# Performance work log

Measured on AMD Instinct MI355X. Metric: run time of the kernel, lower is better.

The kernel has to match this reference:

```python
import jax, jax.numpy as jnp
import numpy as np

NC, K, SD = 8, 1024, 64
L = NC * SD
B = 8192
TAU = 0.07
COMMIT_W = 1.0
CONTRAST_W = 1.0
EPS = 1e-12


def setup_inputs() -> dict:
    key = jax.random.key(0)
    kz, ke = jax.random.split(key)
    z = jax.random.normal(kz, (B, L), dtype=jnp.float32)
    embeddings = jax.random.normal(ke, (NC, K, SD), dtype=jnp.float32)
    return {"z": z, "embeddings": embeddings}


def reference(z, embeddings):
    sg = jax.lax.stop_gradient
    Bn, Ln = z.shape
    nc, k, sd = embeddings.shape
    zr = z.reshape(Bn, nc, sd)  # (B, nc, sd)

    # squared distances via ||z||^2 - 2 z.e + ||e||^2 -> (B, nc, K), avoids (B,nc,K,sd)
    z2 = jnp.sum(zr * zr, axis=-1)[:, :, None]
    e2 = jnp.sum(embeddings * embeddings, axis=-1)[None, :, :]
    cross = jnp.einsum('bnd,nkd->bnk', zr, embeddings)
    dists = z2 - 2.0 * cross + e2
    indices = jnp.argmin(dists, axis=-1)  # (B, nc)

    # codebook gather
    quant_splits = embeddings[jnp.arange(nc)[None, :], indices]  # (B, nc, sd)
    quant_z = quant_splits.reshape(Bn, Ln)

    commit_loss = jnp.mean((sg(quant_z) - z) ** 2)
    embed_loss = jnp.mean((quant_z - sg(z)) ** 2)
    total_commit = commit_loss + embed_loss

    quant_z_st = z + sg(quant_z - z)

    z_norm = z / jnp.maximum(jnp.linalg.norm(z, axis=-1, keepdims=True), EPS)
    q_det = sg(quant_z)
    q_norm = q_det / jnp.maximum(jnp.linalg.norm(q_det, axis=-1, keepdims=True), EPS)
    logits = jnp.matmul(q_norm, z_norm.T) / TAU  # (B, B)
    # cross-entropy with labels = arange(B)
    contrastive = jnp.mean(jax.nn.logsumexp(logits, axis=1) - jnp.diagonal(logits))

    return (quant_z_st, COMMIT_W * total_commit, CONTRAST_W * contrastive, indices)
```

## Files before the change

kernel.cpp:

```cpp
#include <hip/hip_runtime.h>
#include <cstdint>
#include <cstddef>

#define NCB   8
#define KC    1024
#define SDIM  64
#define LDIM  512
#define BATCH 8192
#define INV_TAU (1.0f/0.07f)
#define K2E  20.60992915555662f
#define DBIAS 256.0f

typedef __bf16 bf16_t;
typedef bf16_t bf16x8 __attribute__((ext_vector_type(8)));
typedef float  floatx4 __attribute__((ext_vector_type(4)));
typedef int    intx8  __attribute__((ext_vector_type(8)));
typedef unsigned int u32;

__device__ __forceinline__ unsigned short f2bf(float f) {
    union { float f; unsigned int u; } c; c.f = f;
    unsigned int u = c.u;
    u += 0x7fffu + ((u >> 16) & 1u);
    return (unsigned short)(u >> 16);
}
__device__ __forceinline__ float bf2f(unsigned short h) {
    union { unsigned int u; float f; } c; c.u = ((unsigned int)h) << 16;
    return c.f;
}
__device__ __forceinline__ float exp2_fast(float x) {
    float r; asm("v_exp_f32 %0, %1" : "=v"(r) : "v"(x)); return r;
}
__device__ __forceinline__ void gll16(const void* g, void* l) {
    __builtin_amdgcn_global_load_lds(
        (const __attribute__((address_space(1))) u32*)g,
        (__attribute__((address_space(3))) u32*)l,
        16, 0, 0);
}

__global__ __launch_bounds__(256) void
k_pre(const float* __restrict__ emb, float* __restrict__ e2,
      unsigned short* __restrict__ eh, unsigned short* __restrict__ el,
      float* __restrict__ accs) {
    int id = blockIdx.x * 256 + threadIdx.x;
    const float4* e4 = (const float4*)(emb + (size_t)id * SDIM);
    ushort4* eh4 = (ushort4*)(eh + (size_t)id * SDIM);
    ushort4* el4 = (ushort4*)(el + (size_t)id * SDIM);
    float s0=0.f,s1=0.f,s2=0.f,s3=0.f;
#pragma unroll
    for (int i=0;i<16;i++){ float4 v=e4[i];
        s0=fmaf(v.x,v.x,s0); s1=fmaf(v.y,v.y,s1);
        s2=fmaf(v.z,v.z,s2); s3=fmaf(v.w,v.w,s3);
        ushort4 h, l;
        h.x=f2bf(v.x); l.x=f2bf(v.x-bf2f(h.x));
        h.y=f2bf(v.y); l.y=f2bf(v.y-bf2f(h.y));
        h.z=f2bf(v.z); l.z=f2bf(v.z-bf2f(h.z));
        h.w=f2bf(v.w); l.w=f2bf(v.w-bf2f(h.w));
        eh4[i]=h; el4[i]=l;
    }
    e2[id] = (s0+s1)+(s2+s3);
    if (id==0){ accs[0]=0.f; accs[1]=0.f; accs[2]=0.f; }
}

__device__ __forceinline__ double dist64d(const float* __restrict__ e,
                                          const float* __restrict__ zg) {
    double se=0.0, sz=0.0;
#pragma unroll 8
    for (int i=0;i<64;i++){ double ev=(double)e[i];
        se = fma(ev,ev,se); sz = fma(ev,(double)zg[i],sz); }
    return se - 2.0*sz;
}

__global__ __launch_bounds__(256,3) void
k_argmin(const unsigned short* __restrict__ eh, const unsigned short* __restrict__ el,
         const float* __restrict__ e2, const float* __restrict__ z,
         const float* __restrict__ emb, float* __restrict__ out_q,
         float* __restrict__ out_idx, float* __restrict__ accs) {
    __shared__ __align__(16) unsigned short Bh[2][64*64], Bl[2][64*64];
    __shared__ unsigned int mK[2][128][2];

    const int tid = threadIdx.x;
    const int n   = blockIdx.y;
    const int i0  = blockIdx.x * 128;
    const int wid = tid >> 6, lane = tid & 63;
    const int wm = wid & 1, wn = wid >> 1;
    const int c  = lane & 15, qq = lane >> 4;

    const unsigned char* ehb = (const unsigned char*)(eh + (size_t)n*KC*SDIM);
    const unsigned char* elb = (const unsigned char*)(el + (size_t)n*KC*SDIM);
    const float* e2n = e2 + n*KC;

    const int brow = lane >> 3;
    const int bchk = ((lane & 7)*16) ^ (brow << 4);

    auto stageB = [&](int buf, int j0){
#pragma unroll
        for (int s=0;s<2;s++){
            int r0 = wid*16 + s*8;
            size_t go = (size_t)(j0 + r0 + brow)*128 + bchk;
            gll16(ehb + go, &Bh[buf][r0*64]);
            gll16(elb + go, &Bl[buf][r0*64]);
        }
    };

    stageB(0, 0);

    bf16x8 ah[4][2], al[4][2];
#pragma unroll
    for (int mt=0;mt<4;mt++)
#pragma unroll
        for (int t=0;t<2;t++){
            const float* zr = z + (size_t)(i0 + wm*64 + mt*16 + c)*LDIM
                                + n*SDIM + t*32 + qq*8;
            float4 v0 = *(const float4*)(zr);
            float4 v1 = *(const float4*)(zr + 4);
            ushort4 h0, l0, h1, l1;
            h0.x=f2bf(v0.x); l0.x=f2bf(v0.x-bf2f(h0.x));
            h0.y=f2bf(v0.y); l0.y=f2bf(v0.y-bf2f(h0.y));
            h0.z=f2bf(v0.z); l0.z=f2bf(v0.z-bf2f(h0.z));
            h0.w=f2bf(v0.w); l0.w=f2bf(v0.w-bf2f(h0.w));
            h1.x=f2bf(v1.x); l1.x=f2bf(v1.x-bf2f(h1.x));
            h1.y=f2bf(v1.y); l1.y=f2bf(v1.y-bf2f(h1.y));
            h1.z=f2bf(v1.z); l1.z=f2bf(v1.z-bf2f(h1.z));
            h1.w=f2bf(v1.w); l1.w=f2bf(v1.w-bf2f(h1.w));
            union { bf16x8 v; ushort4 u[2]; } uh, ul;
            uh.u[0]=h0; uh.u[1]=h1; ul.u[0]=l0; ul.u[1]=l1;
            ah[mt][t]=uh.v; al[mt][t]=ul.v;
        }

    unsigned int k1[16], k2[16];
#pragma unroll
    for (int j=0;j<16;j++){ k1[j]=0xFFFFFFFFu; k2[j]=0xFFFFFFFFu; }

    __syncthreads();

    for (int jt=0; jt<16; jt++){
        const int cur = jt & 1, nxt = cur ^ 1;
        const int j0 = jt*64;
        if (jt < 15) stageB(nxt, j0 + 64);

        float e2v[2];
#pragma unroll
        for (int nt=0;nt<2;nt++)
            e2v[nt] = e2n[j0 + wn*32 + nt*16 + c] + DBIAS;

        floatx4 acc[4][2];
#pragma unroll
        for (int mt=0;mt<4;mt++){
            acc[mt][0]=(floatx4){0.f,0.f,0.f,0.f};
            acc[mt][1]=(floatx4){0.f,0.f,0.f,0.f};
        }

#pragma unroll
        for (int t=0;t<2;t++){
            const int axo = (t*32 + qq*8) ^ ((c&7)<<3);
            bf16x8 bh[2], bl[2];
#pragma unroll
            for (int nt=0;nt<2;nt++){
                int ro = (wn*32 + nt*16 + c)*64 + axo;
                bh[nt] = *(const bf16x8*)(&Bh[cur][ro]);
                bl[nt] = *(const bf16x8*)(&Bl[cur][ro]);
            }
#pragma unroll
            for (int mt=0;mt<4;mt++)
#pragma unroll
                for (int nt=0;nt<2;nt++){
                    acc[mt][nt] = __builtin_amdgcn_mfma_f32_16x16x32_bf16(ah[mt][t], bh[nt], acc[mt][nt], 0,0,0);
                    acc[mt][nt] = __builtin_amdgcn_mfma_f32_16x16x32_bf16(ah[mt][t], bl[nt], acc[mt][nt], 0,0,0);
                    acc[mt][nt] = __builtin_amdgcn_mfma_f32_16x16x32_bf16(al[mt][t], bh[nt], acc[mt][nt], 0,0,0);
                }
        }

#pragma unroll
        for (int nt=0;nt<2;nt++){
            const int colb = wn*32 + nt*16 + c;
            unsigned int kidx = (unsigned int)(j0 + colb);
#pragma unroll
            for (int mt=0;mt<4;mt++)
#pragma unroll
                for (int reg=0;reg<4;reg++){
                    float d = fmaf(-2.0f, acc[mt][nt][reg], e2v[nt]);
                    unsigned int key = (__float_as_uint(d) & 0xFFFFFC00u) | kidx;
                    int s = mt*4+reg;
                    unsigned int o1 = k1[s], o2 = k2[s];
                    unsigned int nk2;
                    asm("v_med3_u32 %0, %1, %2, %3" : "=v"(nk2) : "v"(o1), "v"(o2), "v"(key));
                    k2[s] = nk2;
                    k1[s] = min(o1, key);
                }
        }
        __syncthreads();
    }

#pragma unroll
    for (int off=1; off<16; off<<=1){
#pragma unroll
        for (int s=0;s<16;s++){
            unsigned int o1 = __shfl_xor(k1[s], off);
            unsigned int o2 = __shfl_xor(k2[s], off);
            unsigned int n1 = min(k1[s], o1);
            k2[s] = min( max(k1[s], o1), min(k2[s], o2) );
            k1[s] = n1;
        }
    }
    if (c == 0){
#pragma unroll
        for (int s=0;s<16;s++){
            int row = wm*64 + (s>>2)*16 + qq*4 + (s&3);
            mK[wn][row][0] = k1[s]; mK[wn][row][1] = k2[s];
        }
    }
    __syncthreads();

    if (tid < 128){
        int b = i0 + tid;
        unsigned int a1 = mK[0][tid][0], a2 = mK[0][tid][1];
        unsigned int c1 = mK[1][tid][0], c2 = mK[1][tid][1];
        unsigned int f1 = min(a1, c1);
        unsigned int f2 = min( max(a1, c1), min(a2, c2) );
        int ii1 = (int)(f1 & 0x3FFu);
        int ii2 = (int)(f2 & 0x3FFu);
        float d1q = __uint_as_float(f1 & 0xFFFFFC00u);
        float d2q = __uint_as_float(f2 & 0xFFFFFC00u);

        const float* eb = emb + (size_t)n*KC*SDIM;
        const float* zg = z + (size_t)b*LDIM + n*SDIM;
        if (d2q - d1q < 0.08f) {
            double d1 = dist64d(eb + (size_t)ii1*SDIM, zg);
            double d2 = dist64d(eb + (size_t)ii2*SDIM, zg);
            if (d2 < d1 || (d2 == d1 && ii2 < ii1)) ii1 = ii2;
        }

        const float4* q4 = (const float4*)(eb + (size_t)ii1*SDIM);
        const float4* z4 = (const float4*)zg;
        float4* oq = (float4*)(out_q + (size_t)b*LDIM + n*SDIM);
        float cs = 0.f;
#pragma unroll
        for (int i=0;i<16;i++){
            float4 v = q4[i]; float4 zv = z4[i];
            oq[i] = v;
            float d0=v.x-zv.x, d1=v.y-zv.y, d2=v.z-zv.z, d3=v.w-zv.w;
            cs += d0*d0 + d1*d1 + d2*d2 + d3*d3;
        }
        out_idx[b*NCB + n] = (float)ii1;

        for (int off=32; off; off>>=1) cs += __shfl_down(cs, off);
        if ((tid & 63)==0) atomicAdd(&accs[0], cs);
    }
}

__global__ __launch_bounds__(256) void
k_norm(const float* __restrict__ z, const float* __restrict__ q,
       unsigned char* __restrict__ zn8, unsigned char* __restrict__ qn8,
       float* __restrict__ diag) {
    const int b = blockIdx.x, tid = threadIdx.x;
    const size_t base = (size_t)b*LDIM;
    float2 zv = ((const float2*)(z+base))[tid];
    float2 qv = ((const float2*)(q+base))[tid];
    float sz = zv.x*zv.x + zv.y*zv.y;
    float sq = qv.x*qv.x + qv.y*qv.y;
    float sqz= qv.x*zv.x + qv.y*zv.y;
    for (int off=32; off; off>>=1){
        sz+=__shfl_down(sz,off); sq+=__shfl_down(sq,off); sqz+=__shfl_down(sqz,off);
    }
    __shared__ float red[3][4];
    __shared__ float bc[2];
    int w = tid>>6;
    if ((tid&63)==0){ red[0][w]=sz; red[1][w]=sq; red[2][w]=sqz; }
    __syncthreads();
    if (tid==0){
        float tz = red[0][0]+red[0][1]+red[0][2]+red[0][3];
        float tq = red[1][0]+red[1][1]+red[1][2]+red[1][3];
        float tz_q = red[2][0]+red[2][1]+red[2][2]+red[2][3];
        float inz = 1.0f/fmaxf(sqrtf(tz), 1e-12f);
        float inq = 1.0f/fmaxf(sqrtf(tq), 1e-12f);
        bc[0]=inz; bc[1]=inq;
        diag[b] = tz_q*inz*inq*INV_TAU;
    }
    __syncthreads();
    float inz=bc[0], inq=bc[1];
    int pz = __builtin_amdgcn_cvt_pk_fp8_f32(zv.x*inz, zv.y*inz, 0, false);
    int pq = __builtin_amdgcn_cvt_pk_fp8_f32(qv.x*inq, qv.y*inq, 0, false);
    ((unsigned short*)(zn8+base))[tid] = (unsigned short)(pz & 0xffff);
    ((unsigned short*)(qn8+base))[tid] = (unsigned short)(pq & 0xffff);
}

__global__ __launch_bounds__(512,4) void
k_logits(const unsigned char* __restrict__ qn8, const unsigned char* __restrict__ zn8,
         float* __restrict__ Spart) {
    __shared__ __align__(16) unsigned char Bs[2][64*512];
    const int tid  = threadIdx.x;
    const int i0   = blockIdx.x * 128;
    const int chnk = blockIdx.y;
    const int wid  = tid >> 6, lane = tid & 63;
    const int wm = wid & 3, wn = wid >> 2;
    const int c  = lane & 15, qq = lane >> 4;

    const int brow  = lane >> 5;
    const int bchk0 = (lane & 31) * 16;

    auto stageB = [&](int buf, int j0){
#pragma unroll
        for (int s=0;s<4;s++){
            int r0  = wid*8 + s*2;
            int row = r0 + brow;
            gll16(zn8 + (size_t)(j0+row)*LDIM + (bchk0 ^ ((row&7)<<4)),
                  &Bs[buf][r0*512]);
        }
    };

    stageB(0, chnk*1024);

    intx8 af[2][4];
#pragma unroll
    for (int mt=0;mt<2;mt++){
        const unsigned char* ap = qn8 + (size_t)(i0 + wm*32 + mt*16 + c)*LDIM + qq*32;
#pragma unroll
        for (int kc=0;kc<4;kc++){
            union { intx8 v; uint4 h[2]; } u;
            u.h[0] = *(const uint4*)(ap + kc*128);
            u.h[1] = *(const uint4*)(ap + kc*128 + 16);
            af[mt][kc] = u.v;
        }
    }

    float S[8];
#pragma unroll
    for (int i=0;i<8;i++) S[i] = 0.f;

    __syncthreads();

    for (int jt=0;jt<16;jt++){
        const int cur = jt & 1;
        const int j0 = chnk*1024 + jt*64;
        if (jt < 15) stageB(cur^1, j0 + 64);

        floatx4 acc[2][2];
#pragma unroll
        for (int mt=0;mt<2;mt++){
            acc[mt][0]=(floatx4){0.f,0.f,0.f,0.f};
            acc[mt][1]=(floatx4){0.f,0.f,0.f,0.f};
        }

#pragma unroll
        for (int kc=0;kc<4;kc++){
            intx8 bfr[2];
#pragma unroll
            for (int nt=0;nt<2;nt++){
                const int rb = wn*32 + nt*16 + c;
                const unsigned char* p = &Bs[cur][rb*512];
                const int o = kc*128 + qq*32;
                const int x = (rb&7)<<4;
                union { intx8 v; uint4 h[2]; } u;
                u.h[0] = *(const uint4*)(p + (o ^ x));
                u.h[1] = *(const uint4*)(p + ((o + 16) ^ x));
                bfr[nt] = u.v;
            }
#pragma unroll
            for (int mt=0;mt<2;mt++)
#pragma unroll
                for (int nt=0;nt<2;nt++)
                    acc[mt][nt] = __builtin_amdgcn_mfma_scale_f32_16x16x128_f8f6f4(
                        af[mt][kc], bfr[nt], acc[mt][nt],
                        0, 0,
                        0, 127,
                        0, 127);
        }

#pragma unroll
        for (int mt=0;mt<2;mt++)
#pragma unroll
            for (int reg=0;reg<4;reg++){
                float e0 = exp2_fast(fmaf(acc[mt][0][reg], K2E, -K2E));
                float e1 = exp2_fast(fmaf(acc[mt][1][reg], K2E, -K2E));
                S[mt*4+reg] += e0 + e1;
            }
        __syncthreads();
    }

#pragma unroll
    for (int off=1; off<16; off<<=1)
#pragma unroll
        for (int s=0;s<8;s++) S[s] += __shfl_xor(S[s], off);

    if (c == 0){
        const int p = chnk*2 + wn;
#pragma unroll
        for (int mt=0;mt<2;mt++)
#pragma unroll
            for (int reg=0;reg<4;reg++){
                int row = i0 + wm*32 + mt*16 + qq*4 + reg;
                Spart[p*BATCH + row] = S[mt*4+reg];
            }
    }
}

__global__ __launch_bounds__(256) void
k_finalize(const float* __restrict__ Spart, const float* __restrict__ diag,
           float* __restrict__ accs, float* __restrict__ out_s) {
    int r = blockIdx.x*256 + threadIdx.x;
    float Ssum = 0.f;
#pragma unroll
    for (int p=0;p<16;p++) Ssum += Spart[p*BATCH + r];
    float val = INV_TAU + logf(Ssum) - diag[r];
    for (int off=32; off; off>>=1) val += __shfl_down(val, off);
    if ((threadIdx.x & 63)==0) atomicAdd(&accs[1], val);
    __syncthreads();
    if (threadIdx.x == 0){
        __threadfence();
        unsigned int old = __float_as_uint(atomicAdd(&accs[2], 1.0f));
        if (old == __float_as_uint(31.0f)) {
            __threadfence();
            float a0 = atomicAdd(&accs[0], 0.0f);
            float a1 = atomicAdd(&accs[1], 0.0f);
            out_s[0] = 2.0f*a0 / (float)((size_t)BATCH*LDIM);
            out_s[1] = a1 / (float)BATCH;
        }
    }
}

extern "C" void kernel_launch(void* const* d_in, const int* in_sizes, int n_in,
                              void* d_out, int out_size, void* d_ws, size_t ws_size,
                              hipStream_t stream) {
    const float* z   = (const float*)d_in[0];
    const float* emb = (const float*)d_in[1];
    float* out = (float*)d_out;
    float* out_q       = out;
    float* out_scalars = out + 4194304;
    float* out_idx     = out + 4194306;

    float* wsf   = (float*)d_ws;
    float* e2    = wsf;
    float* accs  = wsf + 8192;
    float* diag  = wsf + 8704;
    float* Spart = wsf + 16896;
    unsigned char* qn8 = (unsigned char*)(Spart + 32*BATCH);
    unsigned char* zn8 = qn8 + (size_t)BATCH*LDIM;
    unsigned short* eh = (unsigned short*)(zn8 + (size_t)BATCH*LDIM);
    unsigned short* el = eh + (size_t)NCB*KC*SDIM;

    k_pre    <<<32,          256, 0, stream>>>(emb, e2, eh, el, accs);
    k_argmin <<<dim3(64,8),  256, 0, stream>>>(eh, el, e2, z, emb,
                                               out_q, out_idx, accs);
    k_norm   <<<BATCH,       256, 0, stream>>>(z, out_q, zn8, qn8, diag);
    k_logits <<<dim3(64,8),  512, 0, stream>>>(qn8, zn8, Spart);
    k_finalize<<<32,         256, 0, stream>>>(Spart, diag, accs, out_scalars);
}
```

Before: 184.3 us.

## Restructure argmin, logits, norm and pre kernels for occupancy and parallelism

k_argmin now stages the z hi/lo bf16 split in shared memory instead of registers, uses 32-wide codebook tiles, and caches the e2 values in LDS. k_logits moves to 256-thread blocks with 32-row B tiles and one N-wave layout, which halves the partial sums that k_finalize has to read. k_norm processes one row per wave with wave-level shuffles, and k_pre spreads each embedding row over 8 threads. Together these aim to cut register pressure, raise occupancy, and spread the small kernels across more threads, at the cost of extra LDS reads for the A operand.

```diff
diff --git a/kernel.cpp b/kernel.cpp
--- a/kernel.cpp
+++ b/kernel.cpp
@@ -41,24 +41,26 @@
 k_pre(const float* __restrict__ emb, float* __restrict__ e2,
       unsigned short* __restrict__ eh, unsigned short* __restrict__ el,
       float* __restrict__ accs) {
-    int id = blockIdx.x * 256 + threadIdx.x;
-    const float4* e4 = (const float4*)(emb + (size_t)id * SDIM);
-    ushort4* eh4 = (ushort4*)(eh + (size_t)id * SDIM);
-    ushort4* el4 = (ushort4*)(el + (size_t)id * SDIM);
-    float s0=0.f,s1=0.f,s2=0.f,s3=0.f;
-#pragma unroll
-    for (int i=0;i<16;i++){ float4 v=e4[i];
-        s0=fmaf(v.x,v.x,s0); s1=fmaf(v.y,v.y,s1);
-        s2=fmaf(v.z,v.z,s2); s3=fmaf(v.w,v.w,s3);
-        ushort4 h, l;
-        h.x=f2bf(v.x); l.x=f2bf(v.x-bf2f(h.x));
-        h.y=f2bf(v.y); l.y=f2bf(v.y-bf2f(h.y));
-        h.z=f2bf(v.z); l.z=f2bf(v.z-bf2f(h.z));
-        h.w=f2bf(v.w); l.w=f2bf(v.w-bf2f(h.w));
-        eh4[i]=h; el4[i]=l;
-    }
-    e2[id] = (s0+s1)+(s2+s3);
-    if (id==0){ accs[0]=0.f; accs[1]=0.f; accs[2]=0.f; }
+    int gid = blockIdx.x * 256 + threadIdx.x;
+    int row = gid >> 3, g = gid & 7;
+    const float4* e4 = (const float4*)(emb + (size_t)row*SDIM + g*8);
+    float4 a = e4[0], b = e4[1];
+    union { ushort4 u4[2]; uint4 v; } H, L;
+    H.u4[0].x=f2bf(a.x); L.u4[0].x=f2bf(a.x-bf2f(H.u4[0].x));
+    H.u4[0].y=f2bf(a.y); L.u4[0].y=f2bf(a.y-bf2f(H.u4[0].y));
+    H.u4[0].z=f2bf(a.z); L.u4[0].z=f2bf(a.z-bf2f(H.u4[0].z));
+    H.u4[0].w=f2bf(a.w); L.u4[0].w=f2bf(a.w-bf2f(H.u4[0].w));
+    H.u4[1].x=f2bf(b.x); L.u4[1].x=f2bf(b.x-bf2f(H.u4[1].x));
+    H.u4[1].y=f2bf(b.y); L.u4[1].y=f2bf(b.y-bf2f(H.u4[1].y));
+    H.u4[1].z=f2bf(b.z); L.u4[1].z=f2bf(b.z-bf2f(H.u4[1].z));
+    H.u4[1].w=f2bf(b.w); L.u4[1].w=f2bf(b.w-bf2f(H.u4[1].w));
+    *(uint4*)(eh + (size_t)row*SDIM + g*8) = H.v;
+    *(uint4*)(el + (size_t)row*SDIM + g*8) = L.v;
+    float s = a.x*a.x + a.y*a.y + a.z*a.z + a.w*a.w
+            + b.x*b.x + b.y*b.y + b.z*b.z + b.w*b.w;
+    s += __shfl_xor(s, 1); s += __shfl_xor(s, 2); s += __shfl_xor(s, 4);
+    if (g == 0) e2[row] = s;
+    if (gid == 0){ accs[0]=0.f; accs[1]=0.f; accs[2]=0.f; }
 }
 
 __device__ __forceinline__ double dist64d(const float* __restrict__ e,
@@ -75,7 +77,9 @@
          const float* __restrict__ e2, const float* __restrict__ z,
          const float* __restrict__ emb, float* __restrict__ out_q,
          float* __restrict__ out_idx, float* __restrict__ accs) {
-    __shared__ __align__(16) unsigned short Bh[2][64*64], Bl[2][64*64];
+    __shared__ __align__(16) unsigned short Ah[128*64], Al[128*64];
+    __shared__ __align__(16) unsigned short Bh[2][32*64], Bl[2][32*64];
+    __shared__ float e2s[2][32];
     __shared__ unsigned int mK[2][128][2];
 
     const int tid = threadIdx.x;
@@ -93,39 +97,29 @@
     const int bchk = ((lane & 7)*16) ^ (brow << 4);
 
     auto stageB = [&](int buf, int j0){
-#pragma unroll
-        for (int s=0;s<2;s++){
-            int r0 = wid*16 + s*8;
-            size_t go = (size_t)(j0 + r0 + brow)*128 + bchk;
-            gll16(ehb + go, &Bh[buf][r0*64]);
-            gll16(elb + go, &Bl[buf][r0*64]);
-        }
+        int r0 = wid*8;
+        size_t go = (size_t)(j0 + r0 + brow)*128 + bchk;
+        gll16(ehb + go, &Bh[buf][r0*64]);
+        gll16(elb + go, &Bl[buf][r0*64]);
     };
 
     stageB(0, 0);
-
-    bf16x8 ah[4][2], al[4][2];
-#pragma unroll
-    for (int mt=0;mt<4;mt++)
-#pragma unroll
-        for (int t=0;t<2;t++){
-            const float* zr = z + (size_t)(i0 + wm*64 + mt*16 + c)*LDIM
-                                + n*SDIM + t*32 + qq*8;
-            float4 v0 = *(const float4*)(zr);
-            float4 v1 = *(const float4*)(zr + 4);
-            ushort4 h0, l0, h1, l1;
-            h0.x=f2bf(v0.x); l0.x=f2bf(v0.x-bf2f(h0.x));
-            h0.y=f2bf(v0.y); l0.y=f2bf(v0.y-bf2f(h0.y));
-            h0.z=f2bf(v0.z); l0.z=f2bf(v0.z-bf2f(h0.z));
-            h0.w=f2bf(v0.w); l0.w=f2bf(v0.w-bf2f(h0.w));
-            h1.x=f2bf(v1.x); l1.x=f2bf(v1.x-bf2f(h1.x));
-            h1.y=f2bf(v1.y); l1.y=f2bf(v1.y-bf2f(h1.y));
-            h1.z=f2bf(v1.z); l1.z=f2bf(v1.z-bf2f(h1.z));
-            h1.w=f2bf(v1.w); l1.w=f2bf(v1.w-bf2f(h1.w));
-            union { bf16x8 v; ushort4 u[2]; } uh, ul;
-            uh.u[0]=h0; uh.u[1]=h1; ul.u[0]=l0; ul.u[1]=l1;
-            ah[mt][t]=uh.v; al[mt][t]=ul.v;
-        }
+    if (tid < 32) e2s[0][tid] = e2n[tid] + DBIAS;
+
+#pragma unroll
+    for (int s=0;s<8;s++){
+        int seg = tid + s*256;
+        int r = seg >> 4, sg = seg & 15;
+        float4 v = *(const float4*)(z + (size_t)(i0+r)*LDIM + n*SDIM + sg*4);
+        ushort4 h, l;
+        h.x=f2bf(v.x); l.x=f2bf(v.x-bf2f(h.x));
+        h.y=f2bf(v.y); l.y=f2bf(v.y-bf2f(h.y));
+        h.z=f2bf(v.z); l.z=f2bf(v.z-bf2f(h.z));
+        h.w=f2bf(v.w); l.w=f2bf(v.w-bf2f(h.w));
+        int off = r*64 + ((sg*4) ^ ((r&7)<<3));
+        *(ushort4*)(&Ah[off]) = h;
+        *(ushort4*)(&Al[off]) = l;
+    }
 
     unsigned int k1[16], k2[16];
 #pragma unroll
@@ -133,52 +127,51 @@
 
     __syncthreads();
 
-    for (int jt=0; jt<16; jt++){
+    for (int jt=0; jt<32; jt++){
         const int cur = jt & 1, nxt = cur ^ 1;
-        const int j0 = jt*64;
-        if (jt < 15) stageB(nxt, j0 + 64);
-
-        float e2v[2];
-#pragma unroll
-        for (int nt=0;nt<2;nt++)
-            e2v[nt] = e2n[j0 + wn*32 + nt*16 + c] + DBIAS;
-
-        floatx4 acc[4][2];
-#pragma unroll
-        for (int mt=0;mt<4;mt++){
-            acc[mt][0]=(floatx4){0.f,0.f,0.f,0.f};
-            acc[mt][1]=(floatx4){0.f,0.f,0.f,0.f};
-        }
+        const int j0 = jt*32;
+        float e2r = 0.f;
+        if (jt < 31){
+            stageB(nxt, j0 + 32);
+            if (tid < 32) e2r = e2n[j0 + 32 + tid];
+        }
+
+        floatx4 acc[4];
+#pragma unroll
+        for (int mt=0;mt<4;mt++) acc[mt] = (floatx4){0.f,0.f,0.f,0.f};
 
 #pragma unroll
         for (int t=0;t<2;t++){
             const int axo = (t*32 + qq*8) ^ ((c&7)<<3);
-            bf16x8 bh[2], bl[2];
-#pragma unroll
-            for (int nt=0;nt<2;nt++){
-                int ro = (wn*32 + nt*16 + c)*64 + axo;
-                bh[nt] = *(const bf16x8*)(&Bh[cur][ro]);
-                bl[nt] = *(const bf16x8*)(&Bl[cur][ro]);
-            }
+            bf16x8 ah[4], alo[4], bh, bl;
+            {
+                int ro = (wn*16 + c)*64 + axo;
+                bh = *(const bf16x8*)(&Bh[cur][ro]);
+                bl = *(const bf16x8*)(&Bl[cur][ro]);
+            }
+#pragma unroll
+            for (int mt=0;mt<4;mt++){
+                int ro = (wm*64 + mt*16 + c)*64 + axo;
+                ah[mt]  = *(const bf16x8*)(&Ah[ro]);
+                alo[mt] = *(const bf16x8*)(&Al[ro]);
+            }
+#pragma unroll
+            for (int mt=0;mt<4;mt++){
+                acc[mt] = __builtin_amdgcn_mfma_f32_16x16x32_bf16(ah[mt],  bh, acc[mt], 0,0,0);
+                acc[mt] = __builtin_amdgcn_mfma_f32_16x16x32_bf16(ah[mt],  bl, acc[mt], 0,0,0);
+                acc[mt] = __builtin_amdgcn_mfma_f32_16x16x32_bf16(alo[mt], bh, acc[mt], 0,0,0);
+            }
+        }
+
+        {
+            const int colb = wn*16 + c;
+            float e2v = e2s[cur][colb];
+            unsigned int kidx = (unsigned int)(j0 + colb);
 #pragma unroll
             for (int mt=0;mt<4;mt++)
 #pragma unroll
-                for (int nt=0;nt<2;nt++){
-                    acc[mt][nt] = __builtin_amdgcn_mfma_f32_16x16x32_bf16(ah[mt][t], bh[nt], acc[mt][nt], 0,0,0);
-                    acc[mt][nt] = __builtin_amdgcn_mfma_f32_16x16x32_bf16(ah[mt][t], bl[nt], acc[mt][nt], 0,0,0);
-                    acc[mt][nt] = __builtin_amdgcn_mfma_f32_16x16x32_bf16(al[mt][t], bh[nt], acc[mt][nt], 0,0,0);
-                }
-        }
-
-#pragma unroll
-        for (int nt=0;nt<2;nt++){
-            const int colb = wn*32 + nt*16 + c;
-            unsigned int kidx = (unsigned int)(j0 + colb);
-#pragma unroll
-            for (int mt=0;mt<4;mt++)
-#pragma unroll
                 for (int reg=0;reg<4;reg++){
-                    float d = fmaf(-2.0f, acc[mt][nt][reg], e2v[nt]);
+                    float d = fmaf(-2.0f, acc[mt][reg], e2v);
                     unsigned int key = (__float_as_uint(d) & 0xFFFFFC00u) | kidx;
                     int s = mt*4+reg;
                     unsigned int o1 = k1[s], o2 = k2[s];
@@ -188,6 +181,8 @@
                     k1[s] = min(o1, key);
                 }
         }
+
+        if (jt < 31 && tid < 32) e2s[nxt][tid] = e2r + DBIAS;
         __syncthreads();
     }
 
@@ -252,47 +247,52 @@
 k_norm(const float* __restrict__ z, const float* __restrict__ q,
        unsigned char* __restrict__ zn8, unsigned char* __restrict__ qn8,
        float* __restrict__ diag) {
-    const int b = blockIdx.x, tid = threadIdx.x;
+    const int wid = threadIdx.x >> 6, lane = threadIdx.x & 63;
+    const int b = blockIdx.x*4 + wid;
     const size_t base = (size_t)b*LDIM;
-    float2 zv = ((const float2*)(z+base))[tid];
-    float2 qv = ((const float2*)(q+base))[tid];
-    float sz = zv.x*zv.x + zv.y*zv.y;
-    float sq = qv.x*qv.x + qv.y*qv.y;
-    float sqz= qv.x*zv.x + qv.y*zv.y;
-    for (int off=32; off; off>>=1){
-        sz+=__shfl_down(sz,off); sq+=__shfl_down(sq,off); sqz+=__shfl_down(sqz,off);
-    }
-    __shared__ float red[3][4];
-    __shared__ float bc[2];
-    int w = tid>>6;
-    if ((tid&63)==0){ red[0][w]=sz; red[1][w]=sq; red[2][w]=sqz; }
-    __syncthreads();
-    if (tid==0){
-        float tz = red[0][0]+red[0][1]+red[0][2]+red[0][3];
-        float tq = red[1][0]+red[1][1]+red[1][2]+red[1][3];
-        float tz_q = red[2][0]+red[2][1]+red[2][2]+red[2][3];
-        float inz = 1.0f/fmaxf(sqrtf(tz), 1e-12f);
-        float inq = 1.0f/fmaxf(sqrtf(tq), 1e-12f);
-        bc[0]=inz; bc[1]=inq;
-        diag[b] = tz_q*inz*inq*INV_TAU;
-    }
-    __syncthreads();
-    float inz=bc[0], inq=bc[1];
-    int pz = __builtin_amdgcn_cvt_pk_fp8_f32(zv.x*inz, zv.y*inz, 0, false);
-    int pq = __builtin_amdgcn_cvt_pk_fp8_f32(qv.x*inq, qv.y*inq, 0, false);
-    ((unsigned short*)(zn8+base))[tid] = (unsigned short)(pz & 0xffff);
-    ((unsigned short*)(qn8+base))[tid] = (unsigned short)(pq & 0xffff);
-}
-
-__global__ __launch_bounds__(512,4) void
+    const float4* z4 = (const float4*)(z + base + lane*8);
+    const float4* q4 = (const float4*)(q + base + lane*8);
+    float4 za = z4[0], zb = z4[1];
+    float4 qa = q4[0], qb = q4[1];
+    float sz = za.x*za.x + za.y*za.y + za.z*za.z + za.w*za.w
+             + zb.x*zb.x + zb.y*zb.y + zb.z*zb.z + zb.w*zb.w;
+    float sq = qa.x*qa.x + qa.y*qa.y + qa.z*qa.z + qa.w*qa.w
+             + qb.x*qb.x + qb.y*qb.y + qb.z*qb.z + qb.w*qb.w;
+    float sqz= qa.x*za.x + qa.y*za.y + qa.z*za.z + qa.w*za.w
+             + qb.x*zb.x + qb.y*zb.y + qb.z*zb.z + qb.w*zb.w;
+#pragma unroll
+    for (int off=1; off<64; off<<=1){
+        sz  += __shfl_xor(sz,  off);
+        sq  += __shfl_xor(sq,  off);
+        sqz += __shfl_xor(sqz, off);
+    }
+    float inz = 1.0f/fmaxf(sqrtf(sz), 1e-12f);
+    float inq = 1.0f/fmaxf(sqrtf(sq), 1e-12f);
+    if (lane == 0) diag[b] = sqz*inz*inq*INV_TAU;
+
+    int z0 = __builtin_amdgcn_cvt_pk_fp8_f32(za.x*inz, za.y*inz, 0, false);
+    z0     = __builtin_amdgcn_cvt_pk_fp8_f32(za.z*inz, za.w*inz, z0, true);
+    int z1 = __builtin_amdgcn_cvt_pk_fp8_f32(zb.x*inz, zb.y*inz, 0, false);
+    z1     = __builtin_amdgcn_cvt_pk_fp8_f32(zb.z*inz, zb.w*inz, z1, true);
+    int q0 = __builtin_amdgcn_cvt_pk_fp8_f32(qa.x*inq, qa.y*inq, 0, false);
+    q0     = __builtin_amdgcn_cvt_pk_fp8_f32(qa.z*inq, qa.w*inq, q0, true);
+    int q1 = __builtin_amdgcn_cvt_pk_fp8_f32(qb.x*inq, qb.y*inq, 0, false);
+    q1     = __builtin_amdgcn_cvt_pk_fp8_f32(qb.z*inq, qb.w*inq, q1, true);
+    uint2 uz; uz.x = (unsigned)z0; uz.y = (unsigned)z1;
+    uint2 uq; uq.x = (unsigned)q0; uq.y = (unsigned)q1;
+    *(uint2*)(zn8 + base + lane*8) = uz;
+    *(uint2*)(qn8 + base + lane*8) = uq;
+}
+
+__global__ __launch_bounds__(256,3) void
 k_logits(const unsigned char* __restrict__ qn8, const unsigned char* __restrict__ zn8,
          float* __restrict__ Spart) {
-    __shared__ __align__(16) unsigned char Bs[2][64*512];
+    __shared__ __align__(16) unsigned char Bs[2][32*512];
     const int tid  = threadIdx.x;
     const int i0   = blockIdx.x * 128;
     const int chnk = blockIdx.y;
     const int wid  = tid >> 6, lane = tid & 63;
-    const int wm = wid & 3, wn = wid >> 2;
+    const int wm = wid;
     const int c  = lane & 15, qq = lane >> 4;
 
     const int brow  = lane >> 5;
@@ -322,6 +322,11 @@
             af[mt][kc] = u.v;
         }
     }
+#pragma unroll
+    for (int mt=0;mt<2;mt++)
+#pragma unroll
+        for (int kc=0;kc<4;kc++)
+            asm volatile("" : "+v"(af[mt][kc]));
 
     float S[8];
 #pragma unroll
@@ -329,10 +334,10 @@
 
     __syncthreads();
 
-    for (int jt=0;jt<16;jt++){
+    for (int jt=0;jt<32;jt++){
         const int cur = jt & 1;
-        const int j0 = chnk*1024 + jt*64;
-        if (jt < 15) stageB(cur^1, j0 + 64);
+        const int j0 = chnk*1024 + jt*32;
+        if (jt < 31) stageB(cur^1, j0 + 32);
 
         floatx4 acc[2][2];
 #pragma unroll
@@ -346,7 +351,7 @@
             intx8 bfr[2];
 #pragma unroll
             for (int nt=0;nt<2;nt++){
-                const int rb = wn*32 + nt*16 + c;
+                const int rb = nt*16 + c;
                 const unsigned char* p = &Bs[cur][rb*512];
                 const int o = kc*128 + qq*32;
                 const int x = (rb&7)<<4;
@@ -383,7 +388,7 @@
         for (int s=0;s<8;s++) S[s] += __shfl_xor(S[s], off);
 
     if (c == 0){
-        const int p = chnk*2 + wn;
+        const int p = chnk;
 #pragma unroll
         for (int mt=0;mt<2;mt++)
 #pragma unroll
@@ -400,7 +405,7 @@
     int r = blockIdx.x*256 + threadIdx.x;
     float Ssum = 0.f;
 #pragma unroll
-    for (int p=0;p<16;p++) Ssum += Spart[p*BATCH + r];
+    for (int p=0;p<8;p++) Ssum += Spart[p*BATCH + r];
     float val = INV_TAU + logf(Ssum) - diag[r];
     for (int off=32; off; off>>=1) val += __shfl_down(val, off);
     if ((threadIdx.x & 63)==0) atomicAdd(&accs[1], val);
@@ -438,10 +443,10 @@
     unsigned short* eh = (unsigned short*)(zn8 + (size_t)BATCH*LDIM);
     unsigned short* el = eh + (size_t)NCB*KC*SDIM;
 
-    k_pre    <<<32,          256, 0, stream>>>(emb, e2, eh, el, accs);
+    k_pre    <<<256,         256, 0, stream>>>(emb, e2, eh, el, accs);
     k_argmin <<<dim3(64,8),  256, 0, stream>>>(eh, el, e2, z, emb,
                                                out_q, out_idx, accs);
-    k_norm   <<<BATCH,       256, 0, stream>>>(z, out_q, zn8, qn8, diag);
-    k_logits <<<dim3(64,8),  512, 0, stream>>>(qn8, zn8, Spart);
+    k_norm   <<<2048,        256, 0, stream>>>(z, out_q, zn8, qn8, diag);
+    k_logits <<<dim3(64,8),  256, 0, stream>>>(qn8, zn8, Spart);
     k_finalize<<<32,         256, 0, stream>>>(Spart, diag, accs, out_scalars);
 }
```

Result: faster. 171.5 us (-7.0%).
